# Performance work log

Measured on AMD Instinct MI355X. Metric: run time of the kernel, lower is better.

## Reference

```python
import jax, jax.numpy as jnp
import numpy as np

ALPHA = 0.2          # LeakyReLU negative slope
NEG_BIG = -9e15      # mask fill value from the original code
N, IN_F, OUT_F = 8192, 128, 64


def setup_inputs() -> dict:
    key = jax.random.key(0)
    k1, k2, k3, k4 = jax.random.split(key, 4)
    h = jax.random.normal(k1, (N, IN_F), dtype=jnp.float32)
    adj = jax.random.randint(k2, (N, N), 0, 2, dtype=jnp.int32)
    W = jax.random.normal(k3, (IN_F, OUT_F), dtype=jnp.float32) * 0.1
    a = jax.random.normal(k4, (2 * OUT_F, 1), dtype=jnp.float32) * 0.1
    return {"h": h, "adj": adj, "W": W, "a": a}


def reference(h, adj, W, a):
    # Wh: [N, F]
    Wh = h @ W
    # e_ij = leakyrelu([Wh_i ; Wh_j] . a) = leakyrelu(Wh_i.a1 + Wh_j.a2)
    # (identical math to the original NxNx2F concat, without materializing it)
    a1 = a[:OUT_F, 0]   # [F]
    a2 = a[OUT_F:, 0]   # [F]
    s1 = Wh @ a1        # [N]
    s2 = Wh @ a2        # [N]
    e = jax.nn.leaky_relu(s1[:, None] + s2[None, :], negative_slope=ALPHA)  # [N, N]
    e = jnp.where(adj > 0, e, jnp.float32(NEG_BIG))
    attention = jax.nn.softmax(e, axis=1)
    # dropout is identity at inference (training=False)
    h_prime = attention @ Wh  # [N, F]
    return jax.nn.elu(h_prime)  # concat=True -> elu
```

## Files before the change

### kernel.cpp

```cpp
#include <hip/hip_runtime.h>
#include <hip/hip_bf16.h>

#define N 8192
#define IN_F 128
#define OUT_F 64
#define LRELU_ALPHA 0.2f
#define PAD 520
#define HSTRIDE 132
#define WTSTRIDE 132

typedef __attribute__((ext_vector_type(8))) short short8;
typedef __attribute__((ext_vector_type(4))) float float4v;
typedef __attribute__((ext_vector_type(4))) unsigned short ushortx4;

__device__ __forceinline__ unsigned short bf16_bits(float x) {
  unsigned u = __builtin_bit_cast(unsigned, x);
  u += 0x7fffu + ((u >> 16) & 1u);
  return (unsigned short)(u >> 16);
}

__global__ __launch_bounds__(256) void prep_kernel(
    const float* __restrict__ h, const float* __restrict__ W,
    const float* __restrict__ a, float* __restrict__ s1,
    float* __restrict__ s2, unsigned short* __restrict__ whF) {
  __shared__ float hs[32 * HSTRIDE];
  __shared__ float wt[64 * WTSTRIDE];
  __shared__ float sred[4][4][8][2];
  const int tid = threadIdx.x;
  const int c32 = blockIdx.x;
  const int w = tid >> 6, L = tid & 63;
  const int r16 = L & 15, quad = L >> 4;
  const int d = w * 16 + r16;

  {
    const int row = tid >> 3;
    const int col0 = (tid & 7) * 16;
    const float4* src = (const float4*)(h + (long)(c32 * 32 + row) * IN_F + col0);
#pragma unroll
    for (int i = 0; i < 4; ++i)
      *(float4*)(hs + row * HSTRIDE + col0 + i * 4) = src[i];
  }
  {
    const int dd = tid & 63;
    const int cb = (tid >> 6) * 32;
#pragma unroll 8
    for (int c = 0; c < 32; ++c)
      wt[dd * WTSTRIDE + cb + c] = W[(cb + c) * OUT_F + dd];
  }
  __syncthreads();

  float acc[8] = {0.f, 0.f, 0.f, 0.f, 0.f, 0.f, 0.f, 0.f};
  const float* hb = hs + (quad * 8) * HSTRIDE;
  const float* wr = wt + d * WTSTRIDE;
#pragma unroll 4
  for (int c4 = 0; c4 < IN_F / 4; ++c4) {
    const float4 wv = *(const float4*)(wr + c4 * 4);
#pragma unroll
    for (int j = 0; j < 8; ++j) {
      const float4 hv = *(const float4*)(hb + j * HSTRIDE + c4 * 4);
      acc[j] = fmaf(hv.x, wv.x, acc[j]);
      acc[j] = fmaf(hv.y, wv.y, acc[j]);
      acc[j] = fmaf(hv.z, wv.z, acc[j]);
      acc[j] = fmaf(hv.w, wv.w, acc[j]);
    }
  }

  {
    ushortx4 lo = {bf16_bits(acc[0]), bf16_bits(acc[1]),
                   bf16_bits(acc[2]), bf16_bits(acc[3])};
    ushortx4 hi = {bf16_bits(acc[4]), bf16_bits(acc[5]),
                   bf16_bits(acc[6]), bf16_bits(acc[7])};
    unsigned short* dst = whF + ((long)c32 * 256 + w * 64 + L) * 8;
    *(ushortx4*)(dst) = lo;
    *(ushortx4*)(dst + 4) = hi;
  }

  const float a1d = a[d], a2d = a[OUT_F + d];
  float p1[8], p2[8];
#pragma unroll
  for (int j = 0; j < 8; ++j) { p1[j] = acc[j] * a1d; p2[j] = acc[j] * a2d; }
#pragma unroll
  for (int off = 1; off < 16; off <<= 1) {
#pragma unroll
    for (int j = 0; j < 8; ++j) {
      p1[j] += __shfl_xor(p1[j], off);
      p2[j] += __shfl_xor(p2[j], off);
    }
  }
  if (r16 == 0) {
#pragma unroll
    for (int j = 0; j < 8; ++j) {
      sred[w][quad][j][0] = p1[j];
      sred[w][quad][j][1] = p2[j];
    }
  }
  __syncthreads();
  if (tid < 32) {
    const int q = tid >> 3, j = tid & 7;
    float v1 = 0.f, v2 = 0.f;
#pragma unroll
    for (int ww = 0; ww < 4; ++ww) {
      v1 += sred[ww][q][j][0];
      v2 += sred[ww][q][j][1];
    }
    const int row = c32 * 32 + q * 8 + j;
    s1[row] = v1;
    s2[row] = v2;
  }
}

__device__ __forceinline__ void p_write(unsigned short* pr, int c, int4 av,
                                        float4 s2v, float s1w) {
  float e0 = s1w + s2v.x; e0 = fmaxf(e0, LRELU_ALPHA * e0);
  float e1 = s1w + s2v.y; e1 = fmaxf(e1, LRELU_ALPHA * e1);
  float e2 = s1w + s2v.z; e2 = fmaxf(e2, LRELU_ALPHA * e2);
  float e3 = s1w + s2v.w; e3 = fmaxf(e3, LRELU_ALPHA * e3);
  const float p0 = av.x > 0 ? __expf(e0) : 0.f;
  const float p1 = av.y > 0 ? __expf(e1) : 0.f;
  const float p2 = av.z > 0 ? __expf(e2) : 0.f;
  const float p3 = av.w > 0 ? __expf(e3) : 0.f;
  ushortx4 pk = {bf16_bits(p0), bf16_bits(p1), bf16_bits(p2), bf16_bits(p3)};
  *(ushortx4*)(pr + c) = pk;
}

__global__ __launch_bounds__(512, 4) void gat_kernel(
    const int* __restrict__ adj, const float* __restrict__ s1,
    const float* __restrict__ s2, const unsigned short* __restrict__ whF,
    float* __restrict__ out) {
  __shared__ __align__(16) unsigned short pbuf[2][16][PAD];
  const int tid = threadIdx.x;
  const int w = tid >> 6, L = tid & 63;
  const int r16 = L & 15, quad = L >> 4;
  const int row0 = blockIdx.x * 16;
  const int rA = 2 * w, rB = 2 * w + 1;
  const long arowA = (long)(row0 + rA) * N;
  const long arowB = (long)(row0 + rB) * N;
  const float s1A = s1[row0 + rA];
  const float s1B = s1[row0 + rB];
  const int c = L * 4;

  float4v acc0 = {0.f, 0.f, 0.f, 0.f};
  float4v acc1 = {0.f, 0.f, 0.f, 0.f};
  float4v acc2 = {0.f, 0.f, 0.f, 0.f};
  float4v acc3 = {0.f, 0.f, 0.f, 0.f};
  float4v accD = {0.f, 0.f, 0.f, 0.f};
  const short ONE = (short)0x3F80;
  const short8 ones = {ONE, ONE, ONE, ONE, ONE, ONE, ONE, ONE};

  int4 pA0[2], pA1[2], pB0[2], pB1[2];
  float4 ps0, ps1;

  {
    const int4 a0 = *(const int4*)(adj + arowA + c);
    const int4 a1 = *(const int4*)(adj + arowA + 256 + c);
    const int4 b0 = *(const int4*)(adj + arowB + c);
    const int4 b1 = *(const int4*)(adj + arowB + 256 + c);
    const float4 sv0 = *(const float4*)(s2 + c);
    const float4 sv1 = *(const float4*)(s2 + 256 + c);
    pA0[0] = *(const int4*)(adj + arowA + 512 + c);
    pA1[0] = *(const int4*)(adj + arowA + 512 + 256 + c);
    pB0[0] = *(const int4*)(adj + arowB + 512 + c);
    pB1[0] = *(const int4*)(adj + arowB + 512 + 256 + c);
    pA0[1] = *(const int4*)(adj + arowA + 1024 + c);
    pA1[1] = *(const int4*)(adj + arowA + 1024 + 256 + c);
    pB0[1] = *(const int4*)(adj + arowB + 1024 + c);
    pB1[1] = *(const int4*)(adj + arowB + 1024 + 256 + c);
    ps0 = *(const float4*)(s2 + 512 + c);
    ps1 = *(const float4*)(s2 + 512 + 256 + c);
    p_write(pbuf[0][rA], c, a0, sv0, s1A);
    p_write(pbuf[0][rA], 256 + c, a1, sv1, s1A);
    p_write(pbuf[0][rB], c, b0, sv0, s1B);
    p_write(pbuf[0][rB], 256 + c, b1, sv1, s1B);
  }
  __syncthreads();

#pragma unroll
  for (int it = 0; it < 16; ++it) {
    const int b = it & 1;
    const int s = it & 1;
#pragma unroll
    for (int half = 0; half < 2; ++half) {
      const int cc = w + half * 8;
      const short8 afrag = *(const short8*)(&pbuf[b][r16][cc * 32 + quad * 8]);
      const unsigned short* bp = whF + ((long)(it * 16 + cc) * 256 + L) * 8;
      const short8 b0 = *(const short8*)(bp);
      const short8 b1 = *(const short8*)(bp + 512);
      const short8 b2 = *(const short8*)(bp + 1024);
      const short8 b3 = *(const short8*)(bp + 1536);
      acc0 = __builtin_amdgcn_mfma_f32_16x16x32_bf16(afrag, b0, acc0, 0, 0, 0);
      acc1 = __builtin_amdgcn_mfma_f32_16x16x32_bf16(afrag, b1, acc1, 0, 0, 0);
      acc2 = __builtin_amdgcn_mfma_f32_16x16x32_bf16(afrag, b2, acc2, 0, 0, 0);
      acc3 = __builtin_amdgcn_mfma_f32_16x16x32_bf16(afrag, b3, acc3, 0, 0, 0);
      accD = __builtin_amdgcn_mfma_f32_16x16x32_bf16(afrag, ones, accD, 0, 0, 0);
    }
    if (it < 15) {
      unsigned short* prA = pbuf[b ^ 1][rA];
      unsigned short* prB = pbuf[b ^ 1][rB];
      const long base = (long)(it + 3) * 512 + c;
      p_write(prA, c, pA0[s], ps0, s1A);
      if (it < 13) pA0[s] = *(const int4*)(adj + arowA + base);
      p_write(prA, 256 + c, pA1[s], ps1, s1A);
      if (it < 13) pA1[s] = *(const int4*)(adj + arowA + base + 256);
      p_write(prB, c, pB0[s], ps0, s1B);
      if (it < 13) pB0[s] = *(const int4*)(adj + arowB + base);
      p_write(prB, 256 + c, pB1[s], ps1, s1B);
      if (it < 13) pB1[s] = *(const int4*)(adj + arowB + base + 256);
      if (it < 14) {
        ps0 = *(const float4*)(s2 + (it + 2) * 512 + c);
        ps1 = *(const float4*)(s2 + (it + 2) * 512 + 256 + c);
      }
    }
    __syncthreads();
  }

  float* M = (float*)pbuf;
  if (w >= 4) {
    float* S = M + (w - 4) * 1040;
#pragma unroll
    for (int reg = 0; reg < 4; ++reg) {
      const int r = quad * 4 + reg;
      S[r * 64 + 0 * 16 + r16] = acc0[reg];
      S[r * 64 + 1 * 16 + r16] = acc1[reg];
      S[r * 64 + 2 * 16 + r16] = acc2[reg];
      S[r * 64 + 3 * 16 + r16] = acc3[reg];
      if (r16 == 0) S[1024 + r] = accD[reg];
    }
  }
  __syncthreads();
  if (w < 4) {
    float* S = M + w * 1040;
#pragma unroll
    for (int reg = 0; reg < 4; ++reg) {
      const int r = quad * 4 + reg;
      S[r * 64 + 0 * 16 + r16] += acc0[reg];
      S[r * 64 + 1 * 16 + r16] += acc1[reg];
      S[r * 64 + 2 * 16 + r16] += acc2[reg];
      S[r * 64 + 3 * 16 + r16] += acc3[reg];
      if (r16 == 0) S[1024 + r] += accD[reg];
    }
  }
  __syncthreads();
#pragma unroll
  for (int part = 0; part < 2; ++part) {
    const int e = part * 512 + tid;
    const int r = e >> 6, k = e & 63;
    float Sv = 0.f, Lv = 0.f;
#pragma unroll
    for (int sl = 0; sl < 4; ++sl) {
      Sv += M[sl * 1040 + r * 64 + k];
      Lv += M[sl * 1040 + 1024 + r];
    }
    const float v = Sv / Lv;
    out[(long)(row0 + r) * OUT_F + k] = v > 0.f ? v : expm1f(v);
  }
}

extern "C" void kernel_launch(void* const* d_in, const int* in_sizes, int n_in,
                              void* d_out, int out_size, void* d_ws, size_t ws_size,
                              hipStream_t stream) {
  const float* h = (const float*)d_in[0];
  const int* adj = (const int*)d_in[1];
  const float* W = (const float*)d_in[2];
  const float* a = (const float*)d_in[3];
  float* out = (float*)d_out;

  float* s1 = (float*)d_ws;
  float* s2 = s1 + N;
  unsigned short* whF = (unsigned short*)(s2 + N);

  prep_kernel<<<N / 32, 256, 0, stream>>>(h, W, a, s1, s2, whF);
  gat_kernel<<<N / 16, 512, 0, stream>>>(adj, s1, s2, whF, out);
}
```

Baseline: 384.3 us.

## Halve GAT block to 256 threads, four rows per wave

Each block of 16 rows now runs with 4 waves instead of 8. Each wave produces P for four adjacency rows and does four MFMA k-chunks per iteration. The adjacency prefetch changes from two stages ahead to one stage ahead, and the final cross-wave reduction now combines 2 partial slices instead of 4. The aim is lower per-block sync and reduction overhead and more blocks resident per CU. The cost is more serial work and register pressure per wave, plus a shallower prefetch that may expose adjacency load latency.

```diff
diff --git a/kernel.cpp b/kernel.cpp
--- a/kernel.cpp
+++ b/kernel.cpp
@@ -123,7 +123,7 @@
   *(ushortx4*)(pr + c) = pk;
 }
 
-__global__ __launch_bounds__(512, 4) void gat_kernel(
+__global__ __launch_bounds__(256, 4) void gat_kernel(
     const int* __restrict__ adj, const float* __restrict__ s1,
     const float* __restrict__ s2, const unsigned short* __restrict__ whF,
     float* __restrict__ out) {
@@ -132,12 +132,13 @@
   const int w = tid >> 6, L = tid & 63;
   const int r16 = L & 15, quad = L >> 4;
   const int row0 = blockIdx.x * 16;
-  const int rA = 2 * w, rB = 2 * w + 1;
-  const long arowA = (long)(row0 + rA) * N;
-  const long arowB = (long)(row0 + rB) * N;
-  const float s1A = s1[row0 + rA];
-  const float s1B = s1[row0 + rB];
+  const int r0 = 4 * w;
   const int c = L * 4;
+  const long abase = (long)(row0 + r0) * N;
+
+  float s1r[4];
+#pragma unroll
+  for (int j = 0; j < 4; ++j) s1r[j] = s1[row0 + r0 + j];
 
   float4v acc0 = {0.f, 0.f, 0.f, 0.f};
   float4v acc1 = {0.f, 0.f, 0.f, 0.f};
@@ -147,40 +148,35 @@
   const short ONE = (short)0x3F80;
   const short8 ones = {ONE, ONE, ONE, ONE, ONE, ONE, ONE, ONE};
 
-  int4 pA0[2], pA1[2], pB0[2], pB1[2];
+  int4 pf[4][2];
   float4 ps0, ps1;
 
   {
-    const int4 a0 = *(const int4*)(adj + arowA + c);
-    const int4 a1 = *(const int4*)(adj + arowA + 256 + c);
-    const int4 b0 = *(const int4*)(adj + arowB + c);
-    const int4 b1 = *(const int4*)(adj + arowB + 256 + c);
     const float4 sv0 = *(const float4*)(s2 + c);
     const float4 sv1 = *(const float4*)(s2 + 256 + c);
-    pA0[0] = *(const int4*)(adj + arowA + 512 + c);
-    pA1[0] = *(const int4*)(adj + arowA + 512 + 256 + c);
-    pB0[0] = *(const int4*)(adj + arowB + 512 + c);
-    pB1[0] = *(const int4*)(adj + arowB + 512 + 256 + c);
-    pA0[1] = *(const int4*)(adj + arowA + 1024 + c);
-    pA1[1] = *(const int4*)(adj + arowA + 1024 + 256 + c);
-    pB0[1] = *(const int4*)(adj + arowB + 1024 + c);
-    pB1[1] = *(const int4*)(adj + arowB + 1024 + 256 + c);
+#pragma unroll
+    for (int j = 0; j < 4; ++j) {
+      const int4 a0 = *(const int4*)(adj + abase + (long)j * N + c);
+      const int4 a1 = *(const int4*)(adj + abase + (long)j * N + 256 + c);
+      p_write(pbuf[0][r0 + j], c, a0, sv0, s1r[j]);
+      p_write(pbuf[0][r0 + j], 256 + c, a1, sv1, s1r[j]);
+    }
+#pragma unroll
+    for (int j = 0; j < 4; ++j) {
+      pf[j][0] = *(const int4*)(adj + abase + (long)j * N + 512 + c);
+      pf[j][1] = *(const int4*)(adj + abase + (long)j * N + 512 + 256 + c);
+    }
     ps0 = *(const float4*)(s2 + 512 + c);
     ps1 = *(const float4*)(s2 + 512 + 256 + c);
-    p_write(pbuf[0][rA], c, a0, sv0, s1A);
-    p_write(pbuf[0][rA], 256 + c, a1, sv1, s1A);
-    p_write(pbuf[0][rB], c, b0, sv0, s1B);
-    p_write(pbuf[0][rB], 256 + c, b1, sv1, s1B);
   }
   __syncthreads();
 
 #pragma unroll
   for (int it = 0; it < 16; ++it) {
     const int b = it & 1;
-    const int s = it & 1;
-#pragma unroll
-    for (int half = 0; half < 2; ++half) {
-      const int cc = w + half * 8;
+#pragma unroll
+    for (int half = 0; half < 4; ++half) {
+      const int cc = w + half * 4;
       const short8 afrag = *(const short8*)(&pbuf[b][r16][cc * 32 + quad * 8]);
       const unsigned short* bp = whF + ((long)(it * 16 + cc) * 256 + L) * 8;
       const short8 b0 = *(const short8*)(bp);
@@ -194,28 +190,28 @@
       accD = __builtin_amdgcn_mfma_f32_16x16x32_bf16(afrag, ones, accD, 0, 0, 0);
     }
     if (it < 15) {
-      unsigned short* prA = pbuf[b ^ 1][rA];
-      unsigned short* prB = pbuf[b ^ 1][rB];
-      const long base = (long)(it + 3) * 512 + c;
-      p_write(prA, c, pA0[s], ps0, s1A);
-      if (it < 13) pA0[s] = *(const int4*)(adj + arowA + base);
-      p_write(prA, 256 + c, pA1[s], ps1, s1A);
-      if (it < 13) pA1[s] = *(const int4*)(adj + arowA + base + 256);
-      p_write(prB, c, pB0[s], ps0, s1B);
-      if (it < 13) pB0[s] = *(const int4*)(adj + arowB + base);
-      p_write(prB, 256 + c, pB1[s], ps1, s1B);
-      if (it < 13) pB1[s] = *(const int4*)(adj + arowB + base + 256);
+      const long nbase = (long)(it + 2) * 512 + c;
+#pragma unroll
+      for (int j = 0; j < 4; ++j) {
+        unsigned short* pr = pbuf[b ^ 1][r0 + j];
+        p_write(pr, c, pf[j][0], ps0, s1r[j]);
+        p_write(pr, 256 + c, pf[j][1], ps1, s1r[j]);
+        if (it < 14) {
+          pf[j][0] = *(const int4*)(adj + abase + (long)j * N + nbase);
+          pf[j][1] = *(const int4*)(adj + abase + (long)j * N + nbase + 256);
+        }
+      }
       if (it < 14) {
-        ps0 = *(const float4*)(s2 + (it + 2) * 512 + c);
-        ps1 = *(const float4*)(s2 + (it + 2) * 512 + 256 + c);
+        ps0 = *(const float4*)(s2 + nbase);
+        ps1 = *(const float4*)(s2 + nbase + 256);
       }
     }
     __syncthreads();
   }
 
   float* M = (float*)pbuf;
-  if (w >= 4) {
-    float* S = M + (w - 4) * 1040;
+  if (w >= 2) {
+    float* S = M + (w - 2) * 1040;
 #pragma unroll
     for (int reg = 0; reg < 4; ++reg) {
       const int r = quad * 4 + reg;
@@ -227,7 +223,7 @@
     }
   }
   __syncthreads();
-  if (w < 4) {
+  if (w < 2) {
     float* S = M + w * 1040;
 #pragma unroll
     for (int reg = 0; reg < 4; ++reg) {
@@ -241,12 +237,12 @@
   }
   __syncthreads();
 #pragma unroll
-  for (int part = 0; part < 2; ++part) {
-    const int e = part * 512 + tid;
+  for (int part = 0; part < 4; ++part) {
+    const int e = part * 256 + tid;
     const int r = e >> 6, k = e & 63;
     float Sv = 0.f, Lv = 0.f;
 #pragma unroll
-    for (int sl = 0; sl < 4; ++sl) {
+    for (int sl = 0; sl < 2; ++sl) {
       Sv += M[sl * 1040 + r * 64 + k];
       Lv += M[sl * 1040 + 1024 + r];
     }
@@ -269,5 +265,5 @@
   unsigned short* whF = (unsigned short*)(s2 + N);
 
   prep_kernel<<<N / 32, 256, 0, stream>>>(h, W, a, s1, s2, whF);
-  gat_kernel<<<N / 16, 512, 0, stream>>>(adj, s1, s2, whF, out);
-}
+  gat_kernel<<<N / 16, 256, 0, stream>>>(adj, s1, s2, whF, out);
+}
```

Result: slower. 395.3 us (+2.9%).
